# Performance work log

Measured on AMD Instinct MI355X. Metric: run time of the kernel, lower is better.

Reference implementation:

```python
import jax, jax.numpy as jnp
import numpy as np

D_MODEL = 1024
H = 4
DK = 128   # head_qk_dim (key_dim=512)
DV = 256   # head_v_dim (value_dim=1024)
EPS = 1e-5
SCALE = DK ** -0.5


def setup_inputs() -> dict:
    key = jax.random.key(0)
    ks = jax.random.split(key, 8)
    w = lambda k, i, o: jax.random.normal(k, (i, o), jnp.float32) * (2.0 ** -2.5) * (6.0 / (i + o)) ** 0.5 * 2
    return {
        "x": jax.random.normal(ks[0], (2, 4096, D_MODEL), jnp.float32),
        "Wq": w(ks[1], D_MODEL, H * DK),
        "Wk": w(ks[2], D_MODEL, H * DK),
        "Wv": w(ks[3], D_MODEL, H * DV),
        "Wb": w(ks[4], D_MODEL, H),
        "Wg": w(ks[5], D_MODEL, H * DV),
        "Wo": w(ks[6], H * DV, D_MODEL),
        "norm_w": jnp.ones((DV,), jnp.float32),
    }


def _delta_rule(q, k, v, beta):
    """Delta-rule linear attention. q,k: [b,n,h,dk], v: [b,n,h,dv], beta: [b,n,h].
    S_t = S_{t-1} + k_t (beta_t * (v_t - k_t^T S_{t-1}))^T ; o_t = q_t^T S_t."""
    b = q.shape[0]
    # time-major for scan: [n,b,h,*]
    qt = jnp.moveaxis(q, 1, 0)
    kt = jnp.moveaxis(k, 1, 0)
    vt = jnp.moveaxis(v, 1, 0)
    bt = jnp.moveaxis(beta, 1, 0)
    S0 = jnp.zeros((b, H, DK, DV), q.dtype)

    def step(S, inp):
        q_t, k_t, v_t, b_t = inp
        pred = jnp.einsum('bhk,bhkv->bhv', k_t, S)          # current memory readout
        delta = (v_t - pred) * b_t[..., None]                # beta-scaled error
        S = S + k_t[..., :, None] * delta[..., None, :]      # rank-1 update [b,h,dk,dv]
        o_t = jnp.einsum('bhk,bhkv->bhv', q_t, S)
        return S, o_t

    _, o = jax.lax.scan(step, S0, (qt, kt, vt, bt))          # o: [n,b,h,dv]
    return jnp.moveaxis(o, 0, 1)                             # [b,n,h,dv]


def reference(x, Wq, Wk, Wv, Wb, Wg, Wo, norm_w):
    b, n, _ = x.shape
    q = (x @ Wq).reshape(b, n, H, DK)
    k = (x @ Wk).reshape(b, n, H, DK)
    v = (x @ Wv).reshape(b, n, H, DV)
    beta = jax.nn.sigmoid(x @ Wb)                            # [b,n,h]
    # L2-normalize keys (delta-rule kernels assume unit-norm k) and scale q
    k = k * jax.lax.rsqrt(jnp.sum(k * k, axis=-1, keepdims=True) + 1e-12)
    q = q * SCALE
    o = _delta_rule(q, k, v, beta)                           # [b,n,h,dv]
    # FusedRMSNormSwishGate over head_v_dim
    g = (x @ Wg).reshape(b, n, H, DV)
    o = o * jax.lax.rsqrt(jnp.mean(o * o, axis=-1, keepdims=True) + EPS) * norm_w
    o = o * (g * jax.nn.sigmoid(g))                          # swish gate
    return o.reshape(b, n, H * DV) @ Wo
```

## Files before the change

kernel.cpp:

```cpp
#include <hip/hip_runtime.h>
#include <hip/hip_bf16.h>
#include <stdint.h>
#include <stddef.h>

typedef __attribute__((ext_vector_type(8))) short short8v;
typedef __attribute__((ext_vector_type(4))) float f32x4;
typedef unsigned short us;

__device__ __forceinline__ float bf2f(unsigned short u) {
    return __uint_as_float(((unsigned int)u) << 16);
}
__device__ __forceinline__ unsigned short f2bf(float f) {
    unsigned int x = __float_as_uint(f);
    x += 0x7fffu + ((x >> 16) & 1u);
    return (unsigned short)(x >> 16);
}
__device__ __forceinline__ unsigned int cvtpk(float lo, float hi) {
    unsigned int r;
    asm("v_cvt_pk_bf16_f32 %0, %1, %2" : "=v"(r) : "v"(lo), "v"(hi));
    return r;
}

#define NTOK 8192
#define DM   1024
#define NPROJ 3072
#define SEQ  4096
#define NCHUNK 64
#define SCQ 0.08838834764831845f

#define GLDS16(g, l) __builtin_amdgcn_global_load_lds( \
    (const __attribute__((address_space(1))) void*)(g), \
    (__attribute__((address_space(3))) void*)(l), 16, 0, 0)

__device__ __forceinline__ void bar_lgkm() {
    asm volatile("s_waitcnt lgkmcnt(0)" ::: "memory");
    __builtin_amdgcn_s_barrier();
    __builtin_amdgcn_sched_barrier(0);
}

__device__ __forceinline__ int sw16(int row, int k) {
    int u = k >> 3;
    int us_ = (u & 8) | ((u ^ row) & 7);
    return row * 128 + us_ * 8 + (k & 7);
}
__device__ __forceinline__ int sw8(int row, int k) {
    int u = k >> 3;
    int us_ = (u ^ row) & 7;
    return row * 64 + us_ * 8 + (k & 7);
}
__device__ __forceinline__ int sw128(int row, int k) {
    int u = k >> 3;
    return row * 128 + ((u ^ row) & 15) * 8 + (k & 7);
}
__device__ __forceinline__ int sw64(int row, int k) {
    int u = k >> 3;
    return row * 64 + ((u ^ row) & 7) * 8 + (k & 7);
}
__device__ __forceinline__ int sw64b(int row, int k) {
    int u = k >> 3;
    return row * 64 + ((u ^ row ^ (row >> 3)) & 7) * 8 + (k & 7);
}
__device__ __forceinline__ int swU(int t, int j) {
    int jj = j & 127, u = jj >> 3;
    int us_ = (u & 8) | ((u ^ t) & 7);
    return t * 256 + (j >> 7) * 128 + us_ * 8 + (jj & 7);
}
__device__ __forceinline__ int swU128(int t, int jj) {
    int u = jj >> 3;
    int us_ = (u & 8) | ((u ^ t) & 7);
    return t * 128 + us_ * 8 + (jj & 7);
}

__global__ __launch_bounds__(256) void prep(
    const float* __restrict__ x, us* __restrict__ xb,
    const float* __restrict__ Wb, float* __restrict__ beta,
    const float* __restrict__ Wq, const float* __restrict__ Wk,
    const float* __restrict__ Wv, const float* __restrict__ Wg,
    const float* __restrict__ Wo, us* __restrict__ WT, us* __restrict__ WoT)
{
    __shared__ float smem[64 * 65];
    int tid = threadIdx.x;
    int bid = blockIdx.x;

    if (bid < 4096) {
        int i = bid * 256 + tid;
        int tok = i >> 7;
        int kb = (i >> 3) & 15;
        int u = i & 7;
        int ko = kb * 64 + ((u ^ (tok & 7)) * 8);
        const float4* src = (const float4*)(x + (size_t)tok * 1024 + ko);
        float4 v0 = src[0], v1 = src[1];
        uint4 o;
        o.x = cvtpk(v0.x, v0.y); o.y = cvtpk(v0.z, v0.w);
        o.z = cvtpk(v1.x, v1.y); o.w = cvtpk(v1.z, v1.w);
        *(uint4*)(xb + (size_t)i * 8) = o;
        const float4* wbv = (const float4*)Wb;
        float xs[8] = {v0.x, v0.y, v0.z, v0.w, v1.x, v1.y, v1.z, v1.w};
        float4 s = {0.f, 0.f, 0.f, 0.f};
        #pragma unroll
        for (int e = 0; e < 8; e++) {
            float4 w = wbv[ko + e];
            s.x += xs[e] * w.x; s.y += xs[e] * w.y;
            s.z += xs[e] * w.z; s.w += xs[e] * w.w;
        }
        *(float4*)&smem[tid * 4] = s;
        __syncthreads();
        if (tid < 8) {
            int tp = tid >> 2, h = tid & 3;
            float acc = 0.f;
            for (int j = 0; j < 128; j++) acc += smem[(tp * 128 + j) * 4 + h];
            beta[(size_t)(bid * 2 + tp) * 4 + h] = 1.f / (1.f + __expf(-acc));
        }
        return;
    }

    int lb = bid - 4096;
    const float* srcw; us* dst; int N;
    if (lb < 128)      { srcw = Wq; dst = WT;                    N = 512;  }
    else if (lb < 256) { srcw = Wk; dst = WT + (size_t)512 * DM;  N = 512;  lb -= 128; }
    else if (lb < 512) { srcw = Wv; dst = WT + (size_t)1024 * DM; N = 1024; lb -= 256; }
    else if (lb < 768) { srcw = Wg; dst = WT + (size_t)2048 * DM; N = 1024; lb -= 512; }
    else               { srcw = Wo; dst = WoT;                   N = 1024; lb -= 768; }
    int nbx = N >> 6;
    int n0 = (lb % nbx) * 64, k0 = (lb / nbx) * 64;
    float (*tl)[65] = (float(*)[65])smem;
    int tr = tid >> 6, tc = tid & 63;
    #pragma unroll
    for (int i2 = 0; i2 < 16; i2++) {
        int kk = 4 * i2 + tr;
        tl[kk][tc] = srcw[(size_t)(k0 + kk) * N + n0 + tc];
    }
    __syncthreads();
    int n = tid >> 2, seg = (tid & 3) * 16;
    short8v a, b;
    #pragma unroll
    for (int e = 0; e < 8; e++) {
        a[e] = (short)f2bf(tl[seg + e][n]);
        b[e] = (short)f2bf(tl[seg + 8 + e][n]);
    }
    int n_ = n0 + n;
    int o1 = (tid & 3) * 2, o2_ = o1 + 1;
    us* d = dst + (size_t)n_ * DM + k0;
    *(short8v*)(d + (o1 ^ (n_ & 7)) * 8) = a;
    *(short8v*)(d + (o2_ ^ (n_ & 7)) * 8) = b;
}

template<int OUT_F32>
__global__ __launch_bounds__(256) void gemm_bt(
    const us* __restrict__ A, const us* __restrict__ BT,
    void* __restrict__ C, int M, int N, int K)
{
    __shared__ us As[128][64];
    __shared__ us Bs[128][64];
    int tid = threadIdx.x;
    int wave = tid >> 6, lane = tid & 63;
    int wr = (wave >> 1) * 64, wc = (wave & 1) * 64;
    int fr = lane & 15, fq = lane >> 4;
    int nbx = gridDim.x, nwg = nbx * gridDim.y;
    int wg = blockIdx.y * nbx + blockIdx.x;
    int cpx = nwg >> 3;
    wg = (wg & 7) * cpx + (wg >> 3);
    int m0 = (wg % nbx) * 128, n0 = (wg / nbx) * 128;

    f32x4 acc[4][4];
    #pragma unroll
    for (int i = 0; i < 4; i++)
        #pragma unroll
        for (int j = 0; j < 4; j++) acc[i][j] = (f32x4){0.f, 0.f, 0.f, 0.f};

    int rl = lane >> 3, ul = lane & 7;

    for (int k0 = 0; k0 < K; k0 += 64) {
        #pragma unroll
        for (int i = 0; i < 4; i++) {
            int row = wave * 32 + i * 8 + rl;
            GLDS16(&A[(size_t)(m0 + row) * K + k0 + ul * 8], &As[0][0] + (wave * 32 + i * 8) * 64);
            GLDS16(&BT[(size_t)(n0 + row) * K + k0 + ul * 8], &Bs[0][0] + (wave * 32 + i * 8) * 64);
        }
        __syncthreads();
        #pragma unroll
        for (int kk = 0; kk < 2; kk++) {
            short8v a[4], b[4];
            #pragma unroll
            for (int i = 0; i < 4; i++) {
                int ra = wr + i * 16 + fr;
                a[i] = *(const short8v*)&As[ra][((4 * kk + fq) ^ (ra & 7)) * 8];
                int rb = wc + i * 16 + fr;
                b[i] = *(const short8v*)&Bs[rb][((4 * kk + fq) ^ (rb & 7)) * 8];
            }
            #pragma unroll
            for (int i = 0; i < 4; i++)
                #pragma unroll
                for (int j = 0; j < 4; j++)
                    acc[i][j] = __builtin_amdgcn_mfma_f32_16x16x32_bf16(a[i], b[j], acc[i][j], 0, 0, 0);
        }
        __syncthreads();
    }
    #pragma unroll
    for (int i = 0; i < 4; i++)
        #pragma unroll
        for (int j = 0; j < 4; j++)
            #pragma unroll
            for (int t = 0; t < 4; t++) {
                int row = m0 + wr + i * 16 + fq * 4 + t;
                int col = n0 + wc + j * 16 + fr;
                float val = acc[i][j][t];
                if (OUT_F32) ((float*)C)[(size_t)row * N + col] = val;
                else ((us*)C)[(size_t)row * N + col] = f2bf(val);
            }
}

__global__ __launch_bounds__(256) void chunk_pre(
    const us* __restrict__ QKVG, const float* __restrict__ beta,
    us* __restrict__ Wbuf, us* __restrict__ Ubuf,
    us* __restrict__ Kbuf, us* __restrict__ KTbuf)
{
    __shared__ us Ks[8192];
    __shared__ us KTs[8192];
    __shared__ us VT[8192];
    __shared__ us Tb[4096];
    __shared__ float Af[64][64];
    __shared__ float betas[64];

    int c = blockIdx.x, bh = blockIdx.y;
    int b = bh >> 2, h = bh & 3;
    int tid = threadIdx.x;
    int wv = tid >> 6, ln = tid & 63;
    int fr = ln & 15, fq = ln >> 4;
    int tok0 = b * SEQ + c * 64;
    size_t cb = (size_t)bh * NCHUNK + c;

    #pragma unroll
    for (int r = 0; r < 4; r++) {
        int idx = tid + 256 * r;
        int t = idx >> 4, u = idx & 15;
        short8v kv = *(const short8v*)(QKVG + (size_t)(tok0 + t) * NPROJ + 512 + h * 128 + u * 8);
        *(short8v*)(Ks + sw16(t, u * 8)) = kv;
    }
    if (tid < 64) betas[tid] = beta[(size_t)(tok0 + tid) * 4 + h];
    __syncthreads();

    {
        int t = tid >> 2, p = tid & 3;
        short8v v[4];
        float ss = 0.f;
        #pragma unroll
        for (int uu = 0; uu < 4; uu++) {
            v[uu] = *(const short8v*)(Ks + sw16(t, (p * 4 + uu) * 8));
            #pragma unroll
            for (int e = 0; e < 8; e++) {
                float f = bf2f((unsigned short)v[uu][e]);
                ss += f * f;
            }
        }
        ss += __shfl_xor(ss, 1);
        ss += __shfl_xor(ss, 2);
        float rn = rsqrtf(ss + 1e-12f);
        #pragma unroll
        for (int uu = 0; uu < 4; uu++) {
            short8v o;
            #pragma unroll
            for (int e = 0; e < 8; e++)
                o[e] = (short)f2bf(bf2f((unsigned short)v[uu][e]) * rn);
            *(short8v*)(Ks + sw16(t, (p * 4 + uu) * 8)) = o;
        }
    }
    __syncthreads();

    {
        f32x4 aacc[4];
        #pragma unroll
        for (int jt = 0; jt < 4; jt++) aacc[jt] = (f32x4){0.f, 0.f, 0.f, 0.f};
        #pragma unroll
        for (int ks = 0; ks < 4; ks++) {
            short8v ak = *(const short8v*)(Ks + sw16(16 * wv + fr, 32 * ks + 8 * fq));
            #pragma unroll
            for (int jt = 0; jt < 4; jt++) {
                short8v bk = *(const short8v*)(Ks + sw16(16 * jt + fr, 32 * ks + 8 * fq));
                aacc[jt] = __builtin_amdgcn_mfma_f32_16x16x32_bf16(ak, bk, aacc[jt], 0, 0, 0);
            }
        }
        #pragma unroll
        for (int jt = 0; jt < 4; jt++)
            #pragma unroll
            for (int r = 0; r < 4; r++) {
                int t = 16 * wv + 4 * fq + r, s = 16 * jt + fr;
                if (s < t) Af[t][s] = betas[t] * aacc[jt][r];
            }
    }
    __syncthreads();

    if (wv == 0) {
        int cc = ln;
        for (int tb = 0; tb < 8; tb++) {
            int base = tb * 8;
            float xs[8];
            #pragma unroll
            for (int i = 0; i < 8; i++) {
                int t = base + i;
                float v = Af[t][cc];
                #pragma unroll
                for (int s = 0; s < i; s++)
                    v += Af[t][base + s] * xs[s];
                float xt = (cc < t) ? -v : 0.f;
                xs[i] = xt;
                if (cc < t) Af[t][cc] = xt;
            }
            for (int r = base + 8; r < 64; r += 2) {
                float u0 = 0.f, u1 = 0.f;
                #pragma unroll
                for (int s = 0; s < 8; s++) {
                    float a0 = Af[r][base + s];
                    float a1 = Af[r + 1][base + s];
                    u0 += a0 * xs[s];
                    u1 += a1 * xs[s];
                }
                Af[r][cc] += u0;
                Af[r + 1][cc] += u1;
            }
        }
    } else {
        int q = tid - 64;
        for (int g = q; g < 1024; g += 192) {
            int t = g >> 4, u = g & 15;
            short8v kv = *(const short8v*)(Ks + sw16(t, u * 8));
            #pragma unroll
            for (int e = 0; e < 8; e++)
                KTs[sw64b(u * 8 + e, t)] = (unsigned short)kv[e];
        }
        for (int g = q; g < 1024; g += 192) {
            int t = g >> 4, jg = g & 15;
            short8v vv = *(const short8v*)(QKVG + (size_t)(tok0 + t) * NPROJ + 1024 + h * 256 + jg * 8);
            #pragma unroll
            for (int e = 0; e < 8; e++)
                VT[sw64b(jg * 8 + e, t)] = (unsigned short)vv[e];
        }
    }
    __syncthreads();

    {
        #pragma unroll
        for (int i = 0; i < 4; i++) {
            int idx = tid + 256 * i;
            int t = idx >> 4, u = idx & 15;
            short8v kv = *(const short8v*)(Ks + sw16(t, u * 8));
            *(short8v*)(Kbuf + cb * 8192 + t * 128 + (size_t)(((u ^ t) & 15) * 8)) = kv;
        }
        #pragma unroll
        for (int i = 0; i < 16; i++) {
            int idx = tid + 256 * i;
            int t = idx >> 6, s = idx & 63;
            float tv = (s < t) ? Af[t][s] : (s == t ? 1.f : 0.f);
            Tb[sw8(t, s)] = f2bf(tv * betas[s]);
        }
        #pragma unroll
        for (int i = 0; i < 4; i++) {
            int idx = tid + 256 * i;
            *(short8v*)(KTbuf + cb * 8192 + (size_t)idx * 8) =
                *(const short8v*)(KTs + (size_t)idx * 8);
        }
    }
    __syncthreads();

    {
        f32x4 wacc[8], uacc[8];
        #pragma unroll
        for (int jt = 0; jt < 8; jt++) {
            wacc[jt] = (f32x4){0.f, 0.f, 0.f, 0.f};
            uacc[jt] = (f32x4){0.f, 0.f, 0.f, 0.f};
        }
        #pragma unroll
        for (int ks = 0; ks < 2; ks++) {
            short8v at = *(const short8v*)(Tb + sw8(16 * wv + fr, 32 * ks + 8 * fq));
            #pragma unroll
            for (int jt = 0; jt < 8; jt++) {
                short8v bk = *(const short8v*)(KTs + sw64b(16 * jt + fr, 32 * ks + 8 * fq));
                wacc[jt] = __builtin_amdgcn_mfma_f32_16x16x32_bf16(at, bk, wacc[jt], 0, 0, 0);
                short8v bv = *(const short8v*)(VT + sw64b(16 * jt + fr, 32 * ks + 8 * fq));
                uacc[jt] = __builtin_amdgcn_mfma_f32_16x16x32_bf16(at, bv, uacc[jt], 0, 0, 0);
            }
        }
        #pragma unroll
        for (int jt = 0; jt < 8; jt++)
            #pragma unroll
            for (int r = 0; r < 4; r++) {
                int t = 16 * wv + 4 * fq + r, d = 16 * jt + fr;
                Wbuf[cb * 8192 + (d >> 6) * 4096 + sw64(t, d & 63)] = f2bf(-wacc[jt][r]);
                Ubuf[cb * 16384 + swU(t, d)] = f2bf(uacc[jt][r]);
            }
    }
    __syncthreads();

    #pragma unroll
    for (int i = 0; i < 4; i++) {
        int g = tid + 256 * i;
        int t = g >> 4, jg = g & 15;
        short8v vv = *(const short8v*)(QKVG + (size_t)(tok0 + t) * NPROJ + 1024 + h * 256 + 128 + jg * 8);
        #pragma unroll
        for (int e = 0; e < 8; e++)
            VT[sw64b(jg * 8 + e, t)] = (unsigned short)vv[e];
    }
    __syncthreads();
    {
        f32x4 uacc[8];
        #pragma unroll
        for (int jt = 0; jt < 8; jt++) uacc[jt] = (f32x4){0.f, 0.f, 0.f, 0.f};
        #pragma unroll
        for (int ks = 0; ks < 2; ks++) {
            short8v at = *(const short8v*)(Tb + sw8(16 * wv + fr, 32 * ks + 8 * fq));
            #pragma unroll
            for (int jt = 0; jt < 8; jt++) {
                short8v bv = *(const short8v*)(VT + sw64b(16 * jt + fr, 32 * ks + 8 * fq));
                uacc[jt] = __builtin_amdgcn_mfma_f32_16x16x32_bf16(at, bv, uacc[jt], 0, 0, 0);
            }
        }
        #pragma unroll
        for (int jt = 0; jt < 8; jt++)
            #pragma unroll
            for (int r = 0; r < 4; r++) {
                int t = 16 * wv + 4 * fq + r, j = 16 * jt + fr;
                Ubuf[cb * 16384 + swU(t, 128 + j)] = f2bf(uacc[jt][r]);
            }
    }
}

#define SCW 0
#define SCKT 8192
#define SCU 16384
#define SCBUF 17408
#define SSTB (2 * SCBUF)
#define SDTB (2 * SCBUF + 2048)

__global__ __launch_bounds__(256, 1) void fused_scan_qg(
    const us* __restrict__ xb, const us* __restrict__ WT, us* __restrict__ QKVG,
    const us* __restrict__ Wbuf, const us* __restrict__ Ubuf,
    const us* __restrict__ KTbuf, us* __restrict__ Sbuf)
{
    extern __shared__ us lds[];
    int tid = threadIdx.x;

    if (blockIdx.x < 128) {
        if (tid >= 128) {
            for (int c = 0; c < NCHUNK; c++) __builtin_amdgcn_s_barrier();
            return;
        }
        int wv = tid >> 6, ln = tid & 63;
        int fr = ln & 15, fq = ln >> 4;
        int sl = blockIdx.x >> 3;
        int j0 = sl * 16;
        int bh = blockIdx.x & 7;

        short8v id0;
        #pragma unroll
        for (int e = 0; e < 8; e++)
            id0[e] = (short)((8 * fq + e == fr) ? 0x3F80 : 0);

        f32x4 sacc[4];
        #pragma unroll
        for (int i = 0; i < 4; i++) sacc[i] = (f32x4){0.f, 0.f, 0.f, 0.f};

        us* ST = lds + SSTB + wv * 1024;

        auto issue = [&](int c1) {
            size_t cb = (size_t)bh * NCHUNK + c1;
            us* dst = lds + (c1 & 1) * SCBUF;
            const us* Wc = Wbuf + cb * 8192 + wv * 4096;
            const us* Kc = KTbuf + cb * 8192 + wv * 4096;
            #pragma unroll
            for (int i = 0; i < 8; i++) {
                GLDS16(Wc + i * 512 + ln * 8, dst + SCW + wv * 4096 + i * 512);
                GLDS16(Kc + i * 512 + ln * 8, dst + SCKT + wv * 4096 + i * 512);
            }
            if (wv) {
                const us* Uc = Ubuf + cb * 16384;
                #pragma unroll
                for (int i = 0; i < 2; i++) {
                    int t = i * 32 + (ln >> 1);
                    GLDS16(Uc + swU(t, j0 + (ln & 1) * 8), dst + SCU + i * 512);
                }
            }
        };

        issue(0);

        for (int c = 0; c < NCHUNK; c++) {
            const us* ba = lds + (c & 1) * SCBUF;
            us* DTw = lds + SDTB + (c & 1) * 2048 + wv * 1024;
            const us* DTr = lds + SDTB + (c & 1) * 2048;
            size_t sb = ((size_t)bh * NCHUNK + c) * 32768 + sl * 2048 + wv * 1024;

            #pragma unroll
            for (int dt = 0; dt < 4; dt++) {
                uint2 w;
                w.x = cvtpk(sacc[dt][0], sacc[dt][1]);
                w.y = cvtpk(sacc[dt][2], sacc[dt][3]);
                int dl = 16 * dt + 4 * fq;
                int off = fr * 64 + (((dl >> 3) ^ fr) & 7) * 8 + (dl & 7);
                *(uint2*)&ST[off] = w;
                *(uint2*)(Sbuf + sb + off) = w;
            }
            if (c + 1 < NCHUNK) issue(c + 1);
            if (c + 1 < NCHUNK) {
                if (wv) asm volatile("s_waitcnt vmcnt(22)" ::: "memory");
                else    asm volatile("s_waitcnt vmcnt(20)" ::: "memory");
            } else {
                asm volatile("s_waitcnt vmcnt(4)" ::: "memory");
            }
            __builtin_amdgcn_sched_barrier(0);

            f32x4 dacc[4];
            #pragma unroll
            for (int tt = 0; tt < 4; tt++) dacc[tt] = (f32x4){0.f, 0.f, 0.f, 0.f};
            #pragma unroll
            for (int kc = 0; kc < 2; kc++) {
                short8v bs = *(const short8v*)&ST[fr * 64 + (((4 * kc + fq) ^ fr) & 7) * 8];
                #pragma unroll
                for (int tt = 0; tt < 4; tt++) {
                    short8v aw = *(const short8v*)&ba[SCW + wv * 4096 + sw64(16 * tt + fr, 32 * kc + 8 * fq)];
                    dacc[tt] = __builtin_amdgcn_mfma_f32_16x16x32_bf16(aw, bs, dacc[tt], 0, 0, 0);
                }
            }
            if (wv) {
                #pragma unroll
                for (int tt = 0; tt < 4; tt++) {
                    short8v au = *(const short8v*)&ba[SCU + (16 * tt + fr) * 16 + 8 * (fq & 1)];
                    dacc[tt] = __builtin_amdgcn_mfma_f32_16x16x32_bf16(au, id0, dacc[tt], 0, 0, 0);
                }
            }
            #pragma unroll
            for (int tt = 0; tt < 4; tt++) {
                uint2 w;
                w.x = cvtpk(dacc[tt][0], dacc[tt][1]);
                w.y = cvtpk(dacc[tt][2], dacc[tt][3]);
                int tl = 16 * tt + 4 * fq;
                *(uint2*)&DTw[fr * 64 + (((tl >> 3) ^ fr) & 7) * 8 + (tl & 7)] = w;
            }
            bar_lgkm();
            #pragma unroll
            for (int kc2 = 0; kc2 < 2; kc2++) {
                int o = fr * 64 + (((4 * kc2 + fq) ^ fr) & 7) * 8;
                short8v bd0 = *(const short8v*)&DTr[o];
                short8v bd1 = *(const short8v*)&DTr[1024 + o];
                #pragma unroll
                for (int dt = 0; dt < 4; dt++) {
                    short8v ak = *(const short8v*)&ba[SCKT + sw64b(64 * wv + 16 * dt + fr, 32 * kc2 + 8 * fq)];
                    sacc[dt] = __builtin_amdgcn_mfma_f32_16x16x32_bf16(ak, bd0, sacc[dt], 0, 0, 0);
                    sacc[dt] = __builtin_amdgcn_mfma_f32_16x16x32_bf16(ak, bd1, sacc[dt], 0, 0, 0);
                }
            }
        }
        return;
    }

    {
        us* As = lds;
        us* Bs = lds + 8192;
        int wave = tid >> 6, lane = tid & 63;
        int wr = (wave >> 1) * 64, wc = (wave & 1) * 64;
        int fr = lane & 15, fq = lane >> 4;
        int wg = blockIdx.x - 128;
        wg = (wg & 7) * 96 + (wg >> 3);
        int m0 = (wg % 64) * 128;
        int ntile = wg / 64;
        int n0 = ntile * 128 + (ntile >= 4 ? 1536 : 0);

        f32x4 acc[4][4];
        #pragma unroll
        for (int i = 0; i < 4; i++)
            #pragma unroll
            for (int j = 0; j < 4; j++) acc[i][j] = (f32x4){0.f, 0.f, 0.f, 0.f};

        int rl = lane >> 3, ul = lane & 7;

        for (int k0 = 0; k0 < DM; k0 += 64) {
            #pragma unroll
            for (int i = 0; i < 4; i++) {
                int row = wave * 32 + i * 8 + rl;
                GLDS16(&xb[(size_t)(m0 + row) * DM + k0 + ul * 8], As + (wave * 32 + i * 8) * 64);
                GLDS16(&WT[(size_t)(n0 + row) * DM + k0 + ul * 8], Bs + (wave * 32 + i * 8) * 64);
            }
            __syncthreads();
            #pragma unroll
            for (int kk = 0; kk < 2; kk++) {
                short8v a[4], b[4];
                #pragma unroll
                for (int i = 0; i < 4; i++) {
                    int ra = wr + i * 16 + fr;
                    a[i] = *(const short8v*)&As[ra * 64 + ((4 * kk + fq) ^ (ra & 7)) * 8];
                    int rb = wc + i * 16 + fr;
                    b[i] = *(const short8v*)&Bs[rb * 64 + ((4 * kk + fq) ^ (rb & 7)) * 8];
                }
                #pragma unroll
                for (int i = 0; i < 4; i++)
                    #pragma unroll
                    for (int j = 0; j < 4; j++)
                        acc[i][j] = __builtin_amdgcn_mfma_f32_16x16x32_bf16(a[i], b[j], acc[i][j], 0, 0, 0);
            }
            __syncthreads();
        }
        #pragma unroll
        for (int i = 0; i < 4; i++)
            #pragma unroll
            for (int j = 0; j < 4; j++)
                #pragma unroll
                for (int t = 0; t < 4; t++) {
                    int row = m0 + wr + i * 16 + fq * 4 + t;
                    int col = n0 + wc + j * 16 + fr;
                    QKVG[(size_t)row * NPROJ + col] = f2bf(acc[i][j][t]);
                }
    }
}

#define K2_W 0
#define K2_P 8192
#define K2_U 12288
#define K2_S 20480
#define K2_Q 36864
#define K2_DT 45056
#define K2_K 53248

__global__ __launch_bounds__(256, 1) void out_k(
    const us* __restrict__ QKVG, const us* __restrict__ Wbuf,
    const us* __restrict__ Ubuf, const us* __restrict__ Kbuf,
    const us* __restrict__ Sbuf, us* __restrict__ Ob)
{
    extern __shared__ us lds[];
    int tid = threadIdx.x;
    int wv = tid >> 6, ln = tid & 63;
    int fr = ln & 15, fq = ln >> 4;
    int c = blockIdx.x;
    int bh = blockIdx.y >> 1, jh = blockIdx.y & 1;
    int b = bh >> 2, h = bh & 3;
    int tok0 = b * SEQ + c * 64;
    size_t cb = (size_t)bh * NCHUNK + c;

    short8v id0, id1;
    #pragma unroll
    for (int e = 0; e < 8; e++) {
        id0[e] = (short)((8 * fq + e == fr) ? 0x3F80 : 0);
        id1[e] = (short)((8 * fq + e == fr + 16) ? 0x3F80 : 0);
    }

    #pragma unroll
    for (int i = 0; i < 4; i++) {
        int q = (i * 4 + wv) * 512 + ln * 8;
        GLDS16(Wbuf + cb * 8192 + q, lds + K2_W + (i * 4 + wv) * 512);
    }
    #pragma unroll
    for (int i = 0; i < 4; i++) {
        int q = (i * 4 + wv) * 512 + ln * 8;
        GLDS16(Kbuf + cb * 8192 + q, lds + K2_K + (i * 4 + wv) * 512);
    }
    #pragma unroll
    for (int i = 0; i < 4; i++) {
        int q = (i * 4 + wv) * 512 + ln * 8;
        int t = q >> 7, r = q & 127;
        GLDS16(Ubuf + cb * 16384 + t * 256 + jh * 128 + r, lds + K2_U + (i * 4 + wv) * 512);
    }
    size_t sbase = cb * 32768 + (size_t)jh * 16384;
    #pragma unroll
    for (int i = 0; i < 8; i++) {
        int q = (i * 4 + wv) * 512 + ln * 8;
        GLDS16(Sbuf + sbase + q, lds + K2_S + (i * 4 + wv) * 512);
    }
    short8v qv[4];
    #pragma unroll
    for (int i = 0; i < 4; i++) {
        int idx = tid + 256 * i;
        int t = idx >> 4, u = idx & 15;
        qv[i] = *(const short8v*)(QKVG + (size_t)(tok0 + t) * NPROJ + h * 128 + u * 8);
    }
    #pragma unroll
    for (int i = 0; i < 4; i++) {
        int idx = tid + 256 * i;
        int t = idx >> 4, u = idx & 15;
        *(short8v*)&lds[K2_Q + sw128(t, u * 8)] = qv[i];
    }
    __syncthreads();

    f32x4 dacc[8], oacc[8];
    #pragma unroll
    for (int jt = 0; jt < 8; jt++) {
        dacc[jt] = (f32x4){0.f, 0.f, 0.f, 0.f};
        oacc[jt] = (f32x4){0.f, 0.f, 0.f, 0.f};
    }
    #pragma unroll
    for (int ks = 0; ks < 4; ks++) {
        short8v aw = *(const short8v*)&lds[K2_W + (ks >> 1) * 4096
            + sw64(16 * wv + fr, (ks & 1) * 32 + 8 * fq)];
        short8v aq = *(const short8v*)&lds[K2_Q + sw128(16 * wv + fr, 32 * ks + 8 * fq)];
        #pragma unroll
        for (int jt = 0; jt < 8; jt++) {
            short8v bs = *(const short8v*)&lds[K2_S + jt * 2048 + (ks >> 1) * 1024
                + fr * 64 + ((((ks & 1) * 4 + fq) ^ fr) & 7) * 8];
            dacc[jt] = __builtin_amdgcn_mfma_f32_16x16x32_bf16(aw, bs, dacc[jt], 0, 0, 0);
            oacc[jt] = __builtin_amdgcn_mfma_f32_16x16x32_bf16(aq, bs, oacc[jt], 0, 0, 0);
        }
    }
    #pragma unroll
    for (int ju = 0; ju < 4; ju++) {
        short8v au = *(const short8v*)&lds[K2_U + swU128(16 * wv + fr, 32 * ju + 8 * fq)];
        dacc[2 * ju + 0] = __builtin_amdgcn_mfma_f32_16x16x32_bf16(au, id0, dacc[2 * ju + 0], 0, 0, 0);
        dacc[2 * ju + 1] = __builtin_amdgcn_mfma_f32_16x16x32_bf16(au, id1, dacc[2 * ju + 1], 0, 0, 0);
    }
    {
        f32x4 pacc[4];
        #pragma unroll
        for (int jt2 = 0; jt2 < 4; jt2++) pacc[jt2] = (f32x4){0.f, 0.f, 0.f, 0.f};
        #pragma unroll
        for (int ks = 0; ks < 4; ks++) {
            short8v aq = *(const short8v*)&lds[K2_Q + sw128(16 * wv + fr, 32 * ks + 8 * fq)];
            #pragma unroll
            for (int jt2 = 0; jt2 < 4; jt2++) {
                short8v bk = *(const short8v*)&lds[K2_K + sw128(16 * jt2 + fr, 32 * ks + 8 * fq)];
                pacc[jt2] = __builtin_amdgcn_mfma_f32_16x16x32_bf16(aq, bk, pacc[jt2], 0, 0, 0);
            }
        }
        #pragma unroll
        for (int jt2 = 0; jt2 < 4; jt2++)
            #pragma unroll
            for (int r = 0; r < 4; r++) {
                int t = 16 * wv + 4 * fq + r, s = 16 * jt2 + fr;
                float val = (s <= t) ? pacc[jt2][r] * SCQ : 0.f;
                lds[K2_P + sw64(t, s)] = f2bf(val);
            }
    }
    #pragma unroll
    for (int jt = 0; jt < 8; jt++)
        #pragma unroll
        for (int r = 0; r < 4; r++) oacc[jt][r] *= SCQ;
    #pragma unroll
    for (int jt = 0; jt < 8; jt++) {
        int j = 16 * jt + fr;
        int t0 = 16 * wv + 4 * fq;
        uint2 w;
        w.x = cvtpk(dacc[jt][0], dacc[jt][1]);
        w.y = cvtpk(dacc[jt][2], dacc[jt][3]);
        *(uint2*)&lds[K2_DT + sw64(j, t0)] = w;
    }
    bar_lgkm();

    #pragma unroll
    for (int ks = 0; ks < 2; ks++) {
        short8v ap = *(const short8v*)&lds[K2_P + sw64(16 * wv + fr, 32 * ks + 8 * fq)];
        #pragma unroll
        for (int jt = 0; jt < 8; jt++) {
            short8v bd = *(const short8v*)&lds[K2_DT + sw64(16 * jt + fr, 32 * ks + 8 * fq)];
            oacc[jt] = __builtin_amdgcn_mfma_f32_16x16x32_bf16(ap, bd, oacc[jt], 0, 0, 0);
        }
    }
    us* ob = Ob + (size_t)tok0 * 1024 + h * 256 + jh * 128;
    #pragma unroll
    for (int jt = 0; jt < 8; jt++)
        #pragma unroll
        for (int r = 0; r < 4; r++) {
            int t = 16 * wv + 4 * fq + r;
            ob[(size_t)t * 1024 + 16 * jt + fr] = f2bf(oacc[jt][r]);
        }
}

__global__ __launch_bounds__(256) void gate_norm(const us* __restrict__ Ob,
                                                 const us* __restrict__ QKVG,
                                                 const float* __restrict__ norm_w,
                                                 us* __restrict__ o2)
{
    int gid = blockIdx.x * 4 + (threadIdx.x >> 6);
    int ln = threadIdx.x & 63;
    int tok = gid >> 2, h = gid & 3;
    size_t base = (size_t)tok * 1024 + h * 256 + ln * 4;
    uint2 ov = *(const uint2*)&Ob[base];
    float o0 = bf2f((us)ov.x), o1 = bf2f((us)(ov.x >> 16));
    float o2v = bf2f((us)ov.y), o3 = bf2f((us)(ov.y >> 16));
    float ss = o0 * o0 + o1 * o1 + o2v * o2v + o3 * o3;
    #pragma unroll
    for (int off = 32; off; off >>= 1) ss += __shfl_xor(ss, off);
    float r = rsqrtf(ss * (1.0f / 256.0f) + 1e-5f);
    uint2 gv = *(const uint2*)&QKVG[(size_t)tok * NPROJ + 2048 + h * 256 + ln * 4];
    float g0 = bf2f((us)gv.x), g1 = bf2f((us)(gv.x >> 16));
    float g2 = bf2f((us)gv.y), g3 = bf2f((us)(gv.y >> 16));
    float4 nw = *(const float4*)&norm_w[ln * 4];
    float r0 = o0 * r * nw.x * (g0 / (1.f + __expf(-g0)));
    float r1 = o1 * r * nw.y * (g1 / (1.f + __expf(-g1)));
    float r2 = o2v * r * nw.z * (g2 / (1.f + __expf(-g2)));
    float r3 = o3 * r * nw.w * (g3 / (1.f + __expf(-g3)));
    uint2 w;
    w.x = cvtpk(r0, r1);
    w.y = cvtpk(r2, r3);
    int u = h * 32 + (ln >> 1);
    size_t dsto = (size_t)tok * 1024 + (size_t)(u >> 3) * 64
                + (size_t)(((u & 7) ^ (tok & 7)) * 8) + (ln & 1) * 4;
    *(uint2*)&o2[dsto] = w;
}

extern "C" void kernel_launch(void* const* d_in, const int* in_sizes, int n_in,
                              void* d_out, int out_size, void* d_ws, size_t ws_size,
                              hipStream_t stream) {
    const float* x      = (const float*)d_in[0];
    const float* Wq     = (const float*)d_in[1];
    const float* Wk     = (const float*)d_in[2];
    const float* Wv     = (const float*)d_in[3];
    const float* Wb     = (const float*)d_in[4];
    const float* Wg     = (const float*)d_in[5];
    const float* Wo     = (const float*)d_in[6];
    const float* norm_w = (const float*)d_in[7];
    float* out = (float*)d_out;

    char* ws = (char*)d_ws;
    us*    xb   = (us*)(ws + 0);
    us*    Ob   = (us*)(ws + 0);
    us*    WT   = (us*)(ws + 16777216);
    us*    KTbuf= (us*)(ws + 23068672);
    us*    QKVG = (us*)(ws + 31457280);
    float* beta = (float*)(ws + 81788928);
    us*    Wbuf = (us*)(ws + 81920000);
    us*    Ubuf = (us*)(ws + 90308608);
    us*    o2   = (us*)(ws + 90308608);
    us*    Kbuf = (us*)(ws + 107085824);
    us*    WoT  = (us*)(ws + 115474432);
    us*    Sbuf = (us*)(ws + 117571584);

    (void)hipFuncSetAttribute((const void*)fused_scan_qg,
                              hipFuncAttributeMaxDynamicSharedMemorySize, 81920);
    (void)hipFuncSetAttribute((const void*)out_k,
                              hipFuncAttributeMaxDynamicSharedMemorySize, 122880);

    prep<<<5120, 256, 0, stream>>>(x, xb, Wb, beta, Wq, Wk, Wv, Wg, Wo, WT, WoT);
    gemm_bt<0><<<dim3(64, 12), 256, 0, stream>>>(xb, WT + (size_t)512 * DM,
                                                 (void*)(QKVG + 512), NTOK, NPROJ, DM);
    chunk_pre<<<dim3(NCHUNK, 8), 256, 0, stream>>>(QKVG, beta, Wbuf, Ubuf, Kbuf, KTbuf);
    fused_scan_qg<<<896, 256, 81920, stream>>>(xb, WT, QKVG, Wbuf, Ubuf, KTbuf, Sbuf);
    out_k<<<dim3(NCHUNK, 16), 256, 122880, stream>>>(QKVG, Wbuf, Ubuf, Kbuf, Sbuf, Ob);
    gate_norm<<<NTOK, 256, 0, stream>>>(Ob, QKVG, norm_w, o2);
    gemm_bt<1><<<dim3(64, 8), 256, 0, stream>>>(o2, WoT, (void*)out, NTOK, DM, DM);
}
```

Before: 234.1 us.

## Double-buffer LDS tiles in gemm_bt with prefetch two k-steps ahead

The GEMM main loop now uses two LDS buffers for the A and B tiles and issues direct global-to-LDS loads two iterations ahead. Partial vmcnt waits and raw barriers replace the two __syncthreads per iteration. The aim is to hide global load latency behind MFMA work. In exchange LDS use per block doubles, which may lower occupancy, and correctness depends on the hand-tuned vmcnt counts.

```diff
diff --git a/kernel.cpp b/kernel.cpp
--- a/kernel.cpp
+++ b/kernel.cpp
@@ -150,8 +150,8 @@
     const us* __restrict__ A, const us* __restrict__ BT,
     void* __restrict__ C, int M, int N, int K)
 {
-    __shared__ us As[128][64];
-    __shared__ us Bs[128][64];
+    __shared__ us As[2][128 * 64];
+    __shared__ us Bs[2][128 * 64];
     int tid = threadIdx.x;
     int wave = tid >> 6, lane = tid & 63;
     int wr = (wave >> 1) * 64, wc = (wave & 1) * 64;
@@ -170,23 +170,36 @@
 
     int rl = lane >> 3, ul = lane & 7;
 
-    for (int k0 = 0; k0 < K; k0 += 64) {
+    auto issue = [&](int k0, int bufi) {
         #pragma unroll
         for (int i = 0; i < 4; i++) {
             int row = wave * 32 + i * 8 + rl;
-            GLDS16(&A[(size_t)(m0 + row) * K + k0 + ul * 8], &As[0][0] + (wave * 32 + i * 8) * 64);
-            GLDS16(&BT[(size_t)(n0 + row) * K + k0 + ul * 8], &Bs[0][0] + (wave * 32 + i * 8) * 64);
-        }
-        __syncthreads();
+            GLDS16(&A[(size_t)(m0 + row) * K + k0 + ul * 8], &As[bufi][(wave * 32 + i * 8) * 64]);
+            GLDS16(&BT[(size_t)(n0 + row) * K + k0 + ul * 8], &Bs[bufi][(wave * 32 + i * 8) * 64]);
+        }
+    };
+
+    int NT = K >> 6;
+    issue(0, 0);
+    if (NT > 1) issue(64, 1);
+
+    for (int t = 0; t < NT; t++) {
+        if (t + 1 < NT) asm volatile("s_waitcnt vmcnt(8)" ::: "memory");
+        else            asm volatile("s_waitcnt vmcnt(0)" ::: "memory");
+        __builtin_amdgcn_sched_barrier(0);
+        __builtin_amdgcn_s_barrier();
+        __builtin_amdgcn_sched_barrier(0);
+        const us* as = As[t & 1];
+        const us* bs = Bs[t & 1];
         #pragma unroll
         for (int kk = 0; kk < 2; kk++) {
             short8v a[4], b[4];
             #pragma unroll
             for (int i = 0; i < 4; i++) {
                 int ra = wr + i * 16 + fr;
-                a[i] = *(const short8v*)&As[ra][((4 * kk + fq) ^ (ra & 7)) * 8];
+                a[i] = *(const short8v*)&as[ra * 64 + ((4 * kk + fq) ^ (ra & 7)) * 8];
                 int rb = wc + i * 16 + fr;
-                b[i] = *(const short8v*)&Bs[rb][((4 * kk + fq) ^ (rb & 7)) * 8];
+                b[i] = *(const short8v*)&bs[rb * 64 + ((4 * kk + fq) ^ (rb & 7)) * 8];
             }
             #pragma unroll
             for (int i = 0; i < 4; i++)
@@ -194,8 +207,10 @@
                 for (int j = 0; j < 4; j++)
                     acc[i][j] = __builtin_amdgcn_mfma_f32_16x16x32_bf16(a[i], b[j], acc[i][j], 0, 0, 0);
         }
-        __syncthreads();
-    }
+        bar_lgkm();
+        if (t + 2 < NT) issue((t + 2) * 64, t & 1);
+    }
+
     #pragma unroll
     for (int i = 0; i < 4; i++)
         #pragma unroll
```

After: 234.1 us. No clear change (+0.0%).
